# Kernel optimization log

Measured on AMD Instinct MI355X. Metric: run time of the kernel, lower is better.

Reference implementation:

```python
import jax, jax.numpy as jnp
import numpy as np

B, T, D_IN, H, N_CLASSES = 32, 64, 10000, 200, 2


def setup_inputs() -> dict:
    key = jax.random.key(0)
    ks = jax.random.split(key, 16)
    s_in = 1.0 / np.sqrt(H)  # torch nn.RNN init scale
    def u(k, shape):
        return jax.random.uniform(k, shape, jnp.float32, -s_in, s_in)
    inp = {"x": jax.random.normal(ks[0], (B, T, D_IN), jnp.float32)}
    dims = [D_IN, H, H]
    for l in range(3):
        inp[f"W_ih{l}"] = u(ks[1 + 4 * l], (H, dims[l]))
        inp[f"W_hh{l}"] = u(ks[2 + 4 * l], (H, H))
        inp[f"b_ih{l}"] = u(ks[3 + 4 * l], (H,))
        inp[f"b_hh{l}"] = u(ks[4 + 4 * l], (H,))
    inp["fc_w"] = u(ks[13], (N_CLASSES, H))
    inp["fc_b"] = u(ks[14], (N_CLASSES,))
    return inp


def _rnn_layer(x_seq, W_ih, W_hh, b_ih, b_hh):
    # x_seq: [B, T, D] -> hidden sequence [B, T, H]
    pre = jnp.einsum('btd,hd->bth', x_seq, W_ih) + b_ih + b_hh  # input proj batched over time
    h0 = jnp.zeros((x_seq.shape[0], W_hh.shape[0]), x_seq.dtype)

    def step(h, p_t):
        h_new = jnp.tanh(p_t + h @ W_hh.T)
        return h_new, h_new

    _, hs = jax.lax.scan(step, h0, jnp.swapaxes(pre, 0, 1))  # [T, B, H]
    return jnp.swapaxes(hs, 0, 1)


def reference(x, W_ih0, W_hh0, b_ih0, b_hh0, W_ih1, W_hh1, b_ih1, b_hh1,
              W_ih2, W_hh2, b_ih2, b_hh2, fc_w, fc_b):
    h = _rnn_layer(x, W_ih0, W_hh0, b_ih0, b_hh0)
    h = _rnn_layer(h, W_ih1, W_hh1, b_ih1, b_hh1)
    h = _rnn_layer(h, W_ih2, W_hh2, b_ih2, b_hh2)
    last = h[:, -1, :]  # [B, H]; dropout is identity at inference
    logits = last @ fc_w.T + fc_b  # [B, n_classes]
    return logits
```

## Files before the change

kernel.cpp:

```cpp
#include <hip/hip_runtime.h>
#include <hip/hip_bf16.h>


typedef __bf16  bf16x8 __attribute__((ext_vector_type(8)));
typedef __bf16  bf16x4 __attribute__((ext_vector_type(4)));
typedef float   f32x4  __attribute__((ext_vector_type(4)));

#define HDIM 200
#define BM 64
#define CHUNK_B 26624
#define MFMA(a, b, c) __builtin_amdgcn_mfma_f32_16x16x32_bf16(a, b, c, 0, 0, 0)

__device__ __forceinline__ void glds16(const void* g, void* l) {
    __builtin_amdgcn_global_load_lds(
        (const __attribute__((address_space(1))) unsigned int*)g,
        (__attribute__((address_space(3))) unsigned int*)l, 16, 0, 0);
}

__global__ void pack_all(const float* __restrict__ W0,
                         const float* __restrict__ W1,
                         const float* __restrict__ W2,
                         __bf16* __restrict__ O0,
                         __bf16* __restrict__ O1,
                         __bf16* __restrict__ O2)
{
    const int T0 = 320 * 1664, T1 = 7 * 1664, T2 = 7 * 1664;
    for (int gt = blockIdx.x * blockDim.x + threadIdx.x; gt < T0 + T1 + T2;
         gt += gridDim.x * blockDim.x) {
        const float* W; __bf16* out; int K, g;
        if (gt < T0)           { W = W0; out = O0; K = 10000; g = gt; }
        else if (gt < T0 + T1) { W = W1; out = O1; K = HDIM;  g = gt - T0; }
        else                   { W = W2; out = O2; K = HDIM;  g = gt - T0 - T1; }

        const int kc = g / 1664;
        const int u  = g - kc * 1664;
        const int isLo = (u >= 832);
        const int u2 = isLo ? u - 832 : u;
        const int nt = u2 >> 6;
        const int l  = u2 & 63;
        const int r  = nt * 16 + (l & 15);
        const int k  = kc * 32 + (l >> 4) * 8;
        bf16x8 v;
        if (r < HDIM && k < K) {
            const float* p = W + (size_t)r * K + k;
            float4 a = *(const float4*)p, b = *(const float4*)(p + 4);
            float f[8] = {a.x, a.y, a.z, a.w, b.x, b.y, b.z, b.w};
#pragma unroll
            for (int i = 0; i < 8; ++i) {
                __bf16 h = (__bf16)f[i];
                v[i] = isLo ? (__bf16)(f[i] - (float)h) : h;
            }
        } else {
#pragma unroll
            for (int i = 0; i < 8; ++i) v[i] = (__bf16)0.f;
        }
        *(bf16x8*)&out[(size_t)g * 8] = v;
    }
}

__global__ __launch_bounds__(512, 4)
void gemm_pipe(const float* __restrict__ A, int lda, int K,
               const __bf16* __restrict__ Bpack,
               float* __restrict__ Cbase, int per_split, int ksteps)
{
    __shared__ alignas(16) __bf16 Ab[2][4096];
    __shared__ alignas(16) __bf16 Bb[2][13312];

    const int tid = threadIdx.x;
    const int kc0 = blockIdx.y * ksteps;
    const int m0  = blockIdx.x * BM;
    float* __restrict__ C = Cbase + (size_t)blockIdx.y * per_split;

    const int wv = tid >> 6, lane = tid & 63;
    const int r16 = lane & 15, kg = lane >> 4;
    const int mg = wv & 1, ng = wv >> 1;
    const int nt0 = ng ? 1 + ng * 3 : 0;
    const int ntw = ng ? 3 : 4;
    const int fb  = lane * 8;

    const int a_row = tid >> 3;
    const int a_q   = tid & 7;
    const float* Arow = A + (size_t)(m0 + a_row) * lda + a_q * 4;
    const int a_off = (a_row >> 4) * 512 + ((a_row & 15) + 16 * (a_q >> 1)) * 8
                    + (a_q & 1) * 4;

    f32x4 acc[2][4];
#pragma unroll
    for (int mi = 0; mi < 2; ++mi)
#pragma unroll
        for (int j = 0; j < 4; ++j) acc[mi][j] = (f32x4)0.f;

    float av[4];
    auto loadA = [&](int ks) {
        const int kb = (kc0 + ks) * 32;
        if (kb + a_q * 4 < K) {
            float4 x0 = *(const float4*)(Arow + kb);
            av[0] = x0.x; av[1] = x0.y; av[2] = x0.z; av[3] = x0.w;
        } else {
#pragma unroll
            for (int i = 0; i < 4; ++i) av[i] = 0.f;
        }
    };
    auto issueB = [&](int ks, int buf) {
        const char* src = (const char*)Bpack + (size_t)(kc0 + ks) * CHUNK_B;
        char* dst = (char*)&Bb[buf][0];
#pragma unroll
        for (int r = 0; r < 3; ++r)
            glds16(src + (r * 512 + tid) * 16, dst + (r * 512 + tid) * 16);
        if (tid < 128)
            glds16(src + (1536 + tid) * 16, dst + (1536 + tid) * 16);
    };

    loadA(0);
    issueB(0, 0);

    for (int ks = 0; ks < ksteps; ++ks) {
        const int cur = ks & 1, nxt = cur ^ 1;
        bf16x4 th, tl;
#pragma unroll
        for (int i = 0; i < 4; ++i) {
            __bf16 h = (__bf16)av[i];
            th[i] = h; tl[i] = (__bf16)(av[i] - (float)h);
        }
        *(bf16x4*)&Ab[cur][a_off]        = th;
        *(bf16x4*)&Ab[cur][2048 + a_off] = tl;
        __syncthreads();
        if (ks + 1 < ksteps) { issueB(ks + 1, nxt); loadA(ks + 1); }

        const int ao0 = (mg * 2 + 0) * 512 + fb;
        const int ao1 = (mg * 2 + 1) * 512 + fb;
        bf16x8 ah0 = *(const bf16x8*)&Ab[cur][ao0];
        bf16x8 al0 = *(const bf16x8*)&Ab[cur][2048 + ao0];
        bf16x8 ah1 = *(const bf16x8*)&Ab[cur][ao1];
        bf16x8 al1 = *(const bf16x8*)&Ab[cur][2048 + ao1];
#pragma unroll
        for (int j = 0; j < 4; ++j) {
            if (j < ntw) {
                const int bo = (nt0 + j) * 512 + fb;
                bf16x8 bh = *(const bf16x8*)&Bb[cur][bo];
                bf16x8 bl = *(const bf16x8*)&Bb[cur][6656 + bo];
                acc[0][j] = MFMA(al0, bh, acc[0][j]);
                acc[0][j] = MFMA(ah0, bl, acc[0][j]);
                acc[0][j] = MFMA(ah0, bh, acc[0][j]);
                acc[1][j] = MFMA(al1, bh, acc[1][j]);
                acc[1][j] = MFMA(ah1, bl, acc[1][j]);
                acc[1][j] = MFMA(ah1, bh, acc[1][j]);
            }
        }
    }

#pragma unroll
    for (int mi = 0; mi < 2; ++mi) {
        const int rb = m0 + mg * 32 + mi * 16 + kg * 4;
#pragma unroll
        for (int j = 0; j < 4; ++j) {
            if (j < ntw) {
                const int n = (nt0 + j) * 16 + r16;
                if (n < HDIM)
#pragma unroll
                    for (int r = 0; r < 4; ++r)
                        C[(size_t)(rb + r) * HDIM + n] = acc[mi][j][r];
            }
        }
    }
}

__global__ void reduce_parts(const float* __restrict__ Pp, float* __restrict__ P)
{
    const int i = blockIdx.x * blockDim.x + threadIdx.x;
    if (i < 102400) {
        float4 s = ((const float4*)Pp)[i];
#pragma unroll
        for (int r = 1; r < 16; ++r) {
            float4 v = ((const float4*)Pp)[(size_t)r * 102400 + i];
            s.x += v.x; s.y += v.y; s.z += v.z; s.w += v.w;
        }
        ((float4*)P)[i] = s;
    }
}

__device__ __forceinline__ float fast_tanh(float x) {
    float e = __expf(-2.f * fabsf(x));
    float r = (1.f - e) / (1.f + e);
    return copysignf(r, x);
}

__device__ __forceinline__ void bar_lds() {
    asm volatile("s_waitcnt lgkmcnt(0)" ::: "memory");
    __builtin_amdgcn_s_barrier();
}

__global__ __launch_bounds__(512, 1)
void rnn_rec(const float* __restrict__ pre,
             const float* __restrict__ Whh,
             const float* __restrict__ bih,
             const float* __restrict__ bhh,
             float* __restrict__ Hout)
{
    const int b   = blockIdx.x;
    const int tid = threadIdx.x;

    __shared__ float preS[64 * HDIM];
    __shared__ float h[HDIM];
    __shared__ float bias[HDIM];
    __shared__ float part[10][HDIM];

    {
        const float4* ps = (const float4*)(pre + (size_t)b * 64 * HDIM);
        float4* pd = (float4*)preS;
        for (int i = tid; i < 3200; i += 512) pd[i] = ps[i];
    }

    const bool act = tid < 500;
    const int g  = tid / 10;
    const int s  = tid - g * 10;
    const int n0 = g * 4;
    const int k0 = s * 20;

    float w[80];
    if (act) {
#pragma unroll
        for (int j = 0; j < 4; ++j) {
            const float* wr = Whh + (size_t)(n0 + j) * HDIM + k0;
#pragma unroll
            for (int i = 0; i < 5; ++i) {
                float4 v = *(const float4*)(wr + i * 4);
                w[j * 20 + i * 4 + 0] = v.x; w[j * 20 + i * 4 + 1] = v.y;
                w[j * 20 + i * 4 + 2] = v.z; w[j * 20 + i * 4 + 3] = v.w;
            }
        }
    }
    if (tid < HDIM) { bias[tid] = bih[tid] + bhh[tid]; h[tid] = 0.f; }
    __syncthreads();

    for (int t = 0; t < 64; ++t) {
        if (act) {
            float a0 = 0.f, a1 = 0.f, a2 = 0.f, a3 = 0.f;
#pragma unroll
            for (int i = 0; i < 5; ++i) {
                float4 hv = *(const float4*)&h[k0 + i * 4];
                a0 += w[ 0 + i*4]*hv.x + w[ 1 + i*4]*hv.y + w[ 2 + i*4]*hv.z + w[ 3 + i*4]*hv.w;
                a1 += w[20 + i*4]*hv.x + w[21 + i*4]*hv.y + w[22 + i*4]*hv.z + w[23 + i*4]*hv.w;
                a2 += w[40 + i*4]*hv.x + w[41 + i*4]*hv.y + w[42 + i*4]*hv.z + w[43 + i*4]*hv.w;
                a3 += w[60 + i*4]*hv.x + w[61 + i*4]*hv.y + w[62 + i*4]*hv.z + w[63 + i*4]*hv.w;
            }
            float4 pv = make_float4(a0, a1, a2, a3);
            *(float4*)&part[s][n0] = pv;
        }
        bar_lds();
        if (tid < HDIM) {
            float sum = part[0][tid];
#pragma unroll
            for (int r = 1; r < 10; ++r) sum += part[r][tid];
            float v = fast_tanh(sum + preS[t * HDIM + tid] + bias[tid]);
            h[tid] = v;
            Hout[((size_t)b * 64 + t) * HDIM + tid] = v;
        }
        bar_lds();
    }
}

__global__ void fc_head(const float* __restrict__ Hlast_base,
                        const float* __restrict__ fcw,
                        const float* __restrict__ fcb,
                        float* __restrict__ out)
{
    const int i = threadIdx.x;
    if (i >= 64) return;
    const int b = i >> 1, cls = i & 1;
    const float* hp = Hlast_base + ((size_t)b * 64 + 63) * HDIM;
    const float* fw = fcw + cls * HDIM;
    float s = fcb[cls];
    for (int j = 0; j < HDIM; ++j) s += hp[j] * fw[j];
    out[b * 2 + cls] = s;
}

extern "C" void kernel_launch(void* const* d_in, const int* in_sizes, int n_in,
                              void* d_out, int out_size, void* d_ws, size_t ws_size,
                              hipStream_t stream) {
    const float* x     = (const float*)d_in[0];
    const float* W_ih0 = (const float*)d_in[1];
    const float* W_hh0 = (const float*)d_in[2];
    const float* b_ih0 = (const float*)d_in[3];
    const float* b_hh0 = (const float*)d_in[4];
    const float* W_ih1 = (const float*)d_in[5];
    const float* W_hh1 = (const float*)d_in[6];
    const float* b_ih1 = (const float*)d_in[7];
    const float* b_hh1 = (const float*)d_in[8];
    const float* W_ih2 = (const float*)d_in[9];
    const float* W_hh2 = (const float*)d_in[10];
    const float* b_ih2 = (const float*)d_in[11];
    const float* b_hh2 = (const float*)d_in[12];
    const float* fc_w  = (const float*)d_in[13];
    const float* fc_b  = (const float*)d_in[14];
    float* out = (float*)d_out;

    const size_t PE = (size_t)2048 * HDIM;
    float* P     = (float*)d_ws;
    float* Hbuf  = P + PE;
    float* Hbuf2 = Hbuf + PE;
    float* Ppart = Hbuf2 + PE;
    __bf16* W0p  = (__bf16*)(Ppart + 16 * PE);
    __bf16* W1p  = W0p + (size_t)320 * 13312;
    __bf16* W2p  = W1p + (size_t)7 * 13312;

    pack_all<<<1024, 256, 0, stream>>>(W_ih0, W_ih1, W_ih2, W0p, W1p, W2p);

    gemm_pipe<<<dim3(32, 16), 512, 0, stream>>>(x, 10000, 10000, W0p, Ppart, (int)PE, 20);
    reduce_parts<<<400, 256, 0, stream>>>(Ppart, P);
    rnn_rec<<<32, 512, 0, stream>>>(P, W_hh0, b_ih0, b_hh0, Hbuf);

    gemm_pipe<<<dim3(32, 1), 512, 0, stream>>>(Hbuf, HDIM, HDIM, W1p, P, (int)PE, 7);
    rnn_rec<<<32, 512, 0, stream>>>(P, W_hh1, b_ih1, b_hh1, Hbuf2);

    gemm_pipe<<<dim3(32, 1), 512, 0, stream>>>(Hbuf2, HDIM, HDIM, W2p, P, (int)PE, 7);
    rnn_rec<<<32, 512, 0, stream>>>(P, W_hh2, b_ih2, b_hh2, Hbuf);

    fc_head<<<1, 64, 0, stream>>>(Hbuf, fc_w, fc_b, out);
}
```

Before: 315.5 us.

## Replace split-K partial buffers with atomic accumulation and load A fragments directly

The split-K layer-0 GEMM now accumulates its 16 partial results into P with float atomicAdd. P is zeroed inside the pack kernel, which removes the 16x partial-sum buffer and the separate reduce kernel. The A operand is no longer staged through LDS: each lane loads its own fp32 fragment from global memory and splits it into bf16 hi/lo in registers. This frees LDS and removes the LDS write and read for A. The cost is contended atomics on P, non-deterministic summation order, and redundant A loads across the wave groups that share rows.

```diff
diff --git a/kernel.cpp b/kernel.cpp
--- a/kernel.cpp
+++ b/kernel.cpp
@@ -3,7 +3,6 @@
 
 
 typedef __bf16  bf16x8 __attribute__((ext_vector_type(8)));
-typedef __bf16  bf16x4 __attribute__((ext_vector_type(4)));
 typedef float   f32x4  __attribute__((ext_vector_type(4)));
 
 #define HDIM 200
@@ -22,8 +21,15 @@
                          const float* __restrict__ W2,
                          __bf16* __restrict__ O0,
                          __bf16* __restrict__ O1,
-                         __bf16* __restrict__ O2)
+                         __bf16* __restrict__ O2,
+                         float* __restrict__ P)
 {
+    {
+        const float4 z = make_float4(0.f, 0.f, 0.f, 0.f);
+        for (int i = blockIdx.x * blockDim.x + threadIdx.x; i < 102400;
+             i += gridDim.x * blockDim.x)
+            ((float4*)P)[i] = z;
+    }
     const int T0 = 320 * 1664, T1 = 7 * 1664, T2 = 7 * 1664;
     for (int gt = blockIdx.x * blockDim.x + threadIdx.x; gt < T0 + T1 + T2;
          gt += gridDim.x * blockDim.x) {
@@ -61,15 +67,16 @@
 __global__ __launch_bounds__(512, 4)
 void gemm_pipe(const float* __restrict__ A, int lda, int K,
                const __bf16* __restrict__ Bpack,
-               float* __restrict__ Cbase, int per_split, int ksteps)
+               float* __restrict__ Cbase, int per_split, int ksteps,
+               int atomic_out)
 {
-    __shared__ alignas(16) __bf16 Ab[2][4096];
     __shared__ alignas(16) __bf16 Bb[2][13312];
 
     const int tid = threadIdx.x;
     const int kc0 = blockIdx.y * ksteps;
     const int m0  = blockIdx.x * BM;
-    float* __restrict__ C = Cbase + (size_t)blockIdx.y * per_split;
+    float* __restrict__ C = atomic_out ? Cbase
+                          : Cbase + (size_t)blockIdx.y * per_split;
 
     const int wv = tid >> 6, lane = tid & 63;
     const int r16 = lane & 15, kg = lane >> 4;
@@ -78,11 +85,9 @@
     const int ntw = ng ? 3 : 4;
     const int fb  = lane * 8;
 
-    const int a_row = tid >> 3;
-    const int a_q   = tid & 7;
-    const float* Arow = A + (size_t)(m0 + a_row) * lda + a_q * 4;
-    const int a_off = (a_row >> 4) * 512 + ((a_row & 15) + 16 * (a_q >> 1)) * 8
-                    + (a_q & 1) * 4;
+    const int k8 = kg * 8;
+    const float* Ap0 = A + (size_t)(m0 + mg * 32 + r16) * lda + k8;
+    const float* Ap1 = Ap0 + (size_t)16 * lda;
 
     f32x4 acc[2][4];
 #pragma unroll
@@ -90,15 +95,21 @@
 #pragma unroll
         for (int j = 0; j < 4; ++j) acc[mi][j] = (f32x4)0.f;
 
-    float av[4];
+    float af[16];
     auto loadA = [&](int ks) {
         const int kb = (kc0 + ks) * 32;
-        if (kb + a_q * 4 < K) {
-            float4 x0 = *(const float4*)(Arow + kb);
-            av[0] = x0.x; av[1] = x0.y; av[2] = x0.z; av[3] = x0.w;
+        if (kb + k8 < K) {
+            const float* p0 = Ap0 + kb;
+            const float* p1 = Ap1 + kb;
+            float4 a = *(const float4*)p0, b = *(const float4*)(p0 + 4);
+            float4 c = *(const float4*)p1, d = *(const float4*)(p1 + 4);
+            af[0]=a.x; af[1]=a.y; af[2]=a.z; af[3]=a.w;
+            af[4]=b.x; af[5]=b.y; af[6]=b.z; af[7]=b.w;
+            af[8]=c.x; af[9]=c.y; af[10]=c.z; af[11]=c.w;
+            af[12]=d.x; af[13]=d.y; af[14]=d.z; af[15]=d.w;
         } else {
 #pragma unroll
-            for (int i = 0; i < 4; ++i) av[i] = 0.f;
+            for (int i = 0; i < 16; ++i) af[i] = 0.f;
         }
     };
     auto issueB = [&](int ks, int buf) {
@@ -116,23 +127,17 @@
 
     for (int ks = 0; ks < ksteps; ++ks) {
         const int cur = ks & 1, nxt = cur ^ 1;
-        bf16x4 th, tl;
-#pragma unroll
-        for (int i = 0; i < 4; ++i) {
-            __bf16 h = (__bf16)av[i];
-            th[i] = h; tl[i] = (__bf16)(av[i] - (float)h);
-        }
-        *(bf16x4*)&Ab[cur][a_off]        = th;
-        *(bf16x4*)&Ab[cur][2048 + a_off] = tl;
+        bf16x8 ah0, al0, ah1, al1;
+#pragma unroll
+        for (int i = 0; i < 8; ++i) {
+            __bf16 h0 = (__bf16)af[i];
+            ah0[i] = h0; al0[i] = (__bf16)(af[i] - (float)h0);
+            __bf16 h1 = (__bf16)af[8 + i];
+            ah1[i] = h1; al1[i] = (__bf16)(af[8 + i] - (float)h1);
+        }
         __syncthreads();
         if (ks + 1 < ksteps) { issueB(ks + 1, nxt); loadA(ks + 1); }
 
-        const int ao0 = (mg * 2 + 0) * 512 + fb;
-        const int ao1 = (mg * 2 + 1) * 512 + fb;
-        bf16x8 ah0 = *(const bf16x8*)&Ab[cur][ao0];
-        bf16x8 al0 = *(const bf16x8*)&Ab[cur][2048 + ao0];
-        bf16x8 ah1 = *(const bf16x8*)&Ab[cur][ao1];
-        bf16x8 al1 = *(const bf16x8*)&Ab[cur][2048 + ao1];
 #pragma unroll
         for (int j = 0; j < 4; ++j) {
             if (j < ntw) {
@@ -156,26 +161,20 @@
         for (int j = 0; j < 4; ++j) {
             if (j < ntw) {
                 const int n = (nt0 + j) * 16 + r16;
-                if (n < HDIM)
-#pragma unroll
-                    for (int r = 0; r < 4; ++r)
-                        C[(size_t)(rb + r) * HDIM + n] = acc[mi][j][r];
-            }
-        }
-    }
-}
-
-__global__ void reduce_parts(const float* __restrict__ Pp, float* __restrict__ P)
-{
-    const int i = blockIdx.x * blockDim.x + threadIdx.x;
-    if (i < 102400) {
-        float4 s = ((const float4*)Pp)[i];
-#pragma unroll
-        for (int r = 1; r < 16; ++r) {
-            float4 v = ((const float4*)Pp)[(size_t)r * 102400 + i];
-            s.x += v.x; s.y += v.y; s.z += v.z; s.w += v.w;
-        }
-        ((float4*)P)[i] = s;
+                if (n < HDIM) {
+                    if (atomic_out) {
+#pragma unroll
+                        for (int r = 0; r < 4; ++r)
+                            atomicAdd(&C[(size_t)(rb + r) * HDIM + n],
+                                      acc[mi][j][r]);
+                    } else {
+#pragma unroll
+                        for (int r = 0; r < 4; ++r)
+                            C[(size_t)(rb + r) * HDIM + n] = acc[mi][j][r];
+                    }
+                }
+            }
+        }
     }
 }
 
@@ -299,21 +298,19 @@
     float* P     = (float*)d_ws;
     float* Hbuf  = P + PE;
     float* Hbuf2 = Hbuf + PE;
-    float* Ppart = Hbuf2 + PE;
-    __bf16* W0p  = (__bf16*)(Ppart + 16 * PE);
+    __bf16* W0p  = (__bf16*)(Hbuf2 + PE);
     __bf16* W1p  = W0p + (size_t)320 * 13312;
     __bf16* W2p  = W1p + (size_t)7 * 13312;
 
-    pack_all<<<1024, 256, 0, stream>>>(W_ih0, W_ih1, W_ih2, W0p, W1p, W2p);
-
-    gemm_pipe<<<dim3(32, 16), 512, 0, stream>>>(x, 10000, 10000, W0p, Ppart, (int)PE, 20);
-    reduce_parts<<<400, 256, 0, stream>>>(Ppart, P);
+    pack_all<<<1024, 256, 0, stream>>>(W_ih0, W_ih1, W_ih2, W0p, W1p, W2p, P);
+
+    gemm_pipe<<<dim3(32, 16), 512, 0, stream>>>(x, 10000, 10000, W0p, P, (int)PE, 20, 1);
     rnn_rec<<<32, 512, 0, stream>>>(P, W_hh0, b_ih0, b_hh0, Hbuf);
 
-    gemm_pipe<<<dim3(32, 1), 512, 0, stream>>>(Hbuf, HDIM, HDIM, W1p, P, (int)PE, 7);
+    gemm_pipe<<<dim3(32, 1), 512, 0, stream>>>(Hbuf, HDIM, HDIM, W1p, P, (int)PE, 7, 0);
     rnn_rec<<<32, 512, 0, stream>>>(P, W_hh1, b_ih1, b_hh1, Hbuf2);
 
-    gemm_pipe<<<dim3(32, 1), 512, 0, stream>>>(Hbuf2, HDIM, HDIM, W2p, P, (int)PE, 7);
+    gemm_pipe<<<dim3(32, 1), 512, 0, stream>>>(Hbuf2, HDIM, HDIM, W2p, P, (int)PE, 7, 0);
     rnn_rec<<<32, 512, 0, stream>>>(P, W_hh2, b_ih2, b_hh2, Hbuf);
 
     fc_head<<<1, 64, 0, stream>>>(Hbuf, fc_w, fc_b, out);
```

After: 348.0 us. +10.3%, slower.

## Fuse all stages into one cooperative persistent kernel with grid syncs

Applied to the files above, without the earlier changes.

Replaces the nine separate launches (pack, big GEMM, reduce, three recurrences, two small GEMMs, FC head) with a single cooperative kernel. Stages are separated by grid-wide syncs, and shared memory is unioned across stages. This aims to remove per-launch overhead and inter-kernel gaps. In exchange it adds grid-sync cost, raises per-block LDS use, which limits occupancy, and runs the GEMM at a different occupancy than its original launch bounds.

```diff
diff --git a/kernel.cpp b/kernel.cpp
--- a/kernel.cpp
+++ b/kernel.cpp
@@ -1,5 +1,8 @@
 #include <hip/hip_runtime.h>
 #include <hip/hip_bf16.h>
+#include <hip/hip_cooperative_groups.h>
+
+namespace cg = cooperative_groups;
 
 
 typedef __bf16  bf16x8 __attribute__((ext_vector_type(8)));
@@ -17,60 +20,34 @@
         (__attribute__((address_space(3))) unsigned int*)l, 16, 0, 0);
 }
 
-__global__ void pack_all(const float* __restrict__ W0,
-                         const float* __restrict__ W1,
-                         const float* __restrict__ W2,
-                         __bf16* __restrict__ O0,
-                         __bf16* __restrict__ O1,
-                         __bf16* __restrict__ O2)
+__device__ __forceinline__ float fast_tanh(float x) {
+    float e = __expf(-2.f * fabsf(x));
+    float r = (1.f - e) / (1.f + e);
+    return copysignf(r, x);
+}
+
+__device__ __forceinline__ void bar_lds() {
+    asm volatile("s_waitcnt lgkmcnt(0)" ::: "memory");
+    __builtin_amdgcn_s_barrier();
+}
+
+struct MegaArgs {
+    const float *x;
+    const float *Wih0, *Whh0, *bih0, *bhh0;
+    const float *Wih1, *Whh1, *bih1, *bhh1;
+    const float *Wih2, *Whh2, *bih2, *bhh2;
+    const float *fcw, *fcb;
+    float *out;
+    float *P, *Hbuf, *Hbuf2, *Ppart;
+    __bf16 *W0p, *W1p, *W2p;
+};
+
+__device__ __noinline__ void gemm_job(
+    const float* __restrict__ A, int lda, int K,
+    const __bf16* __restrict__ Bpack, float* __restrict__ C,
+    int ksteps, int kc0, int m0,
+    __bf16* Ab, __bf16* Bb, int tid)
 {
-    const int T0 = 320 * 1664, T1 = 7 * 1664, T2 = 7 * 1664;
-    for (int gt = blockIdx.x * blockDim.x + threadIdx.x; gt < T0 + T1 + T2;
-         gt += gridDim.x * blockDim.x) {
-        const float* W; __bf16* out; int K, g;
-        if (gt < T0)           { W = W0; out = O0; K = 10000; g = gt; }
-        else if (gt < T0 + T1) { W = W1; out = O1; K = HDIM;  g = gt - T0; }
-        else                   { W = W2; out = O2; K = HDIM;  g = gt - T0 - T1; }
-
-        const int kc = g / 1664;
-        const int u  = g - kc * 1664;
-        const int isLo = (u >= 832);
-        const int u2 = isLo ? u - 832 : u;
-        const int nt = u2 >> 6;
-        const int l  = u2 & 63;
-        const int r  = nt * 16 + (l & 15);
-        const int k  = kc * 32 + (l >> 4) * 8;
-        bf16x8 v;
-        if (r < HDIM && k < K) {
-            const float* p = W + (size_t)r * K + k;
-            float4 a = *(const float4*)p, b = *(const float4*)(p + 4);
-            float f[8] = {a.x, a.y, a.z, a.w, b.x, b.y, b.z, b.w};
-#pragma unroll
-            for (int i = 0; i < 8; ++i) {
-                __bf16 h = (__bf16)f[i];
-                v[i] = isLo ? (__bf16)(f[i] - (float)h) : h;
-            }
-        } else {
-#pragma unroll
-            for (int i = 0; i < 8; ++i) v[i] = (__bf16)0.f;
-        }
-        *(bf16x8*)&out[(size_t)g * 8] = v;
-    }
-}
-
-__global__ __launch_bounds__(512, 4)
-void gemm_pipe(const float* __restrict__ A, int lda, int K,
-               const __bf16* __restrict__ Bpack,
-               float* __restrict__ Cbase, int per_split, int ksteps)
-{
-    __shared__ alignas(16) __bf16 Ab[2][4096];
-    __shared__ alignas(16) __bf16 Bb[2][13312];
-
-    const int tid = threadIdx.x;
-    const int kc0 = blockIdx.y * ksteps;
-    const int m0  = blockIdx.x * BM;
-    float* __restrict__ C = Cbase + (size_t)blockIdx.y * per_split;
-
     const int wv = tid >> 6, lane = tid & 63;
     const int r16 = lane & 15, kg = lane >> 4;
     const int mg = wv & 1, ng = wv >> 1;
@@ -103,7 +80,7 @@
     };
     auto issueB = [&](int ks, int buf) {
         const char* src = (const char*)Bpack + (size_t)(kc0 + ks) * CHUNK_B;
-        char* dst = (char*)&Bb[buf][0];
+        char* dst = (char*)Bb + (size_t)buf * CHUNK_B;
 #pragma unroll
         for (int r = 0; r < 3; ++r)
             glds16(src + (r * 512 + tid) * 16, dst + (r * 512 + tid) * 16);
@@ -122,23 +99,23 @@
             __bf16 h = (__bf16)av[i];
             th[i] = h; tl[i] = (__bf16)(av[i] - (float)h);
         }
-        *(bf16x4*)&Ab[cur][a_off]        = th;
-        *(bf16x4*)&Ab[cur][2048 + a_off] = tl;
+        *(bf16x4*)&Ab[cur * 4096 + a_off]        = th;
+        *(bf16x4*)&Ab[cur * 4096 + 2048 + a_off] = tl;
         __syncthreads();
         if (ks + 1 < ksteps) { issueB(ks + 1, nxt); loadA(ks + 1); }
 
         const int ao0 = (mg * 2 + 0) * 512 + fb;
         const int ao1 = (mg * 2 + 1) * 512 + fb;
-        bf16x8 ah0 = *(const bf16x8*)&Ab[cur][ao0];
-        bf16x8 al0 = *(const bf16x8*)&Ab[cur][2048 + ao0];
-        bf16x8 ah1 = *(const bf16x8*)&Ab[cur][ao1];
-        bf16x8 al1 = *(const bf16x8*)&Ab[cur][2048 + ao1];
+        bf16x8 ah0 = *(const bf16x8*)&Ab[cur * 4096 + ao0];
+        bf16x8 al0 = *(const bf16x8*)&Ab[cur * 4096 + 2048 + ao0];
+        bf16x8 ah1 = *(const bf16x8*)&Ab[cur * 4096 + ao1];
+        bf16x8 al1 = *(const bf16x8*)&Ab[cur * 4096 + 2048 + ao1];
 #pragma unroll
         for (int j = 0; j < 4; ++j) {
             if (j < ntw) {
                 const int bo = (nt0 + j) * 512 + fb;
-                bf16x8 bh = *(const bf16x8*)&Bb[cur][bo];
-                bf16x8 bl = *(const bf16x8*)&Bb[cur][6656 + bo];
+                bf16x8 bh = *(const bf16x8*)&Bb[cur * 13312 + bo];
+                bf16x8 bl = *(const bf16x8*)&Bb[cur * 13312 + 6656 + bo];
                 acc[0][j] = MFMA(al0, bh, acc[0][j]);
                 acc[0][j] = MFMA(ah0, bl, acc[0][j]);
                 acc[0][j] = MFMA(ah0, bh, acc[0][j]);
@@ -163,48 +140,16 @@
             }
         }
     }
-}
-
-__global__ void reduce_parts(const float* __restrict__ Pp, float* __restrict__ P)
+    __syncthreads();
+}
+
+__device__ __noinline__ void rec_job(
+    const float* __restrict__ pre, const float* __restrict__ Whh,
+    const float* __restrict__ bih, const float* __restrict__ bhh,
+    float* __restrict__ Hout, int b, int tid,
+    float* __restrict__ preS, float* __restrict__ hS,
+    float* __restrict__ bias, float* __restrict__ part)
 {
-    const int i = blockIdx.x * blockDim.x + threadIdx.x;
-    if (i < 102400) {
-        float4 s = ((const float4*)Pp)[i];
-#pragma unroll
-        for (int r = 1; r < 16; ++r) {
-            float4 v = ((const float4*)Pp)[(size_t)r * 102400 + i];
-            s.x += v.x; s.y += v.y; s.z += v.z; s.w += v.w;
-        }
-        ((float4*)P)[i] = s;
-    }
-}
-
-__device__ __forceinline__ float fast_tanh(float x) {
-    float e = __expf(-2.f * fabsf(x));
-    float r = (1.f - e) / (1.f + e);
-    return copysignf(r, x);
-}
-
-__device__ __forceinline__ void bar_lds() {
-    asm volatile("s_waitcnt lgkmcnt(0)" ::: "memory");
-    __builtin_amdgcn_s_barrier();
-}
-
-__global__ __launch_bounds__(512, 1)
-void rnn_rec(const float* __restrict__ pre,
-             const float* __restrict__ Whh,
-             const float* __restrict__ bih,
-             const float* __restrict__ bhh,
-             float* __restrict__ Hout)
-{
-    const int b   = blockIdx.x;
-    const int tid = threadIdx.x;
-
-    __shared__ float preS[64 * HDIM];
-    __shared__ float h[HDIM];
-    __shared__ float bias[HDIM];
-    __shared__ float part[10][HDIM];
-
     {
         const float4* ps = (const float4*)(pre + (size_t)b * 64 * HDIM);
         float4* pd = (float4*)preS;
@@ -230,7 +175,7 @@
             }
         }
     }
-    if (tid < HDIM) { bias[tid] = bih[tid] + bhh[tid]; h[tid] = 0.f; }
+    if (tid < HDIM) { bias[tid] = bih[tid] + bhh[tid]; hS[tid] = 0.f; }
     __syncthreads();
 
     for (int t = 0; t < 64; ++t) {
@@ -238,83 +183,158 @@
             float a0 = 0.f, a1 = 0.f, a2 = 0.f, a3 = 0.f;
 #pragma unroll
             for (int i = 0; i < 5; ++i) {
-                float4 hv = *(const float4*)&h[k0 + i * 4];
+                float4 hv = *(const float4*)&hS[k0 + i * 4];
                 a0 += w[ 0 + i*4]*hv.x + w[ 1 + i*4]*hv.y + w[ 2 + i*4]*hv.z + w[ 3 + i*4]*hv.w;
                 a1 += w[20 + i*4]*hv.x + w[21 + i*4]*hv.y + w[22 + i*4]*hv.z + w[23 + i*4]*hv.w;
                 a2 += w[40 + i*4]*hv.x + w[41 + i*4]*hv.y + w[42 + i*4]*hv.z + w[43 + i*4]*hv.w;
                 a3 += w[60 + i*4]*hv.x + w[61 + i*4]*hv.y + w[62 + i*4]*hv.z + w[63 + i*4]*hv.w;
             }
             float4 pv = make_float4(a0, a1, a2, a3);
-            *(float4*)&part[s][n0] = pv;
+            *(float4*)&part[s * HDIM + n0] = pv;
         }
         bar_lds();
         if (tid < HDIM) {
-            float sum = part[0][tid];
-#pragma unroll
-            for (int r = 1; r < 10; ++r) sum += part[r][tid];
+            float sum = part[0 * HDIM + tid];
+#pragma unroll
+            for (int r = 1; r < 10; ++r) sum += part[r * HDIM + tid];
             float v = fast_tanh(sum + preS[t * HDIM + tid] + bias[tid]);
-            h[tid] = v;
+            hS[tid] = v;
             Hout[((size_t)b * 64 + t) * HDIM + tid] = v;
         }
         bar_lds();
     }
-}
-
-__global__ void fc_head(const float* __restrict__ Hlast_base,
-                        const float* __restrict__ fcw,
-                        const float* __restrict__ fcb,
-                        float* __restrict__ out)
+    __syncthreads();
+}
+
+__global__ __launch_bounds__(512, 2)
+void mega(MegaArgs a)
 {
-    const int i = threadIdx.x;
-    if (i >= 64) return;
-    const int b = i >> 1, cls = i & 1;
-    const float* hp = Hlast_base + ((size_t)b * 64 + 63) * HDIM;
-    const float* fw = fcw + cls * HDIM;
-    float s = fcb[cls];
-    for (int j = 0; j < HDIM; ++j) s += hp[j] * fw[j];
-    out[b * 2 + cls] = s;
+    __shared__ alignas(16) char U[69632];
+    __bf16* Ab   = (__bf16*)U;
+    __bf16* Bb   = (__bf16*)(U + 16384);
+    float*  preS = (float*)U;
+    float*  hS   = (float*)(U + 51200);
+    float*  bias = (float*)(U + 52000);
+    float*  part = (float*)(U + 52800);
+
+    const int tid = threadIdx.x;
+    const int bid = blockIdx.x;
+    const int nb  = gridDim.x;
+    cg::grid_group grd = cg::this_grid();
+
+    {
+        const int T0 = 320 * 1664, T1 = 7 * 1664, T2 = 7 * 1664;
+        for (int gt = bid * 512 + tid; gt < T0 + T1 + T2; gt += nb * 512) {
+            const float* W; __bf16* outp; int K, g;
+            if (gt < T0)           { W = a.Wih0; outp = a.W0p; K = 10000; g = gt; }
+            else if (gt < T0 + T1) { W = a.Wih1; outp = a.W1p; K = HDIM;  g = gt - T0; }
+            else                   { W = a.Wih2; outp = a.W2p; K = HDIM;  g = gt - T0 - T1; }
+            const int kc = g / 1664;
+            const int u  = g - kc * 1664;
+            const int isLo = (u >= 832);
+            const int u2 = isLo ? u - 832 : u;
+            const int nt = u2 >> 6;
+            const int l  = u2 & 63;
+            const int r  = nt * 16 + (l & 15);
+            const int k  = kc * 32 + (l >> 4) * 8;
+            bf16x8 v;
+            if (r < HDIM && k < K) {
+                const float* p = W + (size_t)r * K + k;
+                float4 aa = *(const float4*)p, bb = *(const float4*)(p + 4);
+                float f[8] = {aa.x, aa.y, aa.z, aa.w, bb.x, bb.y, bb.z, bb.w};
+#pragma unroll
+                for (int i = 0; i < 8; ++i) {
+                    __bf16 h = (__bf16)f[i];
+                    v[i] = isLo ? (__bf16)(f[i] - (float)h) : h;
+                }
+            } else {
+#pragma unroll
+                for (int i = 0; i < 8; ++i) v[i] = (__bf16)0.f;
+            }
+            *(bf16x8*)&outp[(size_t)g * 8] = v;
+        }
+    }
+    grd.sync();
+
+    for (int job = bid; job < 32 * 16; job += nb) {
+        const int mb = job & 31, ys = job >> 5;
+        gemm_job(a.x, 10000, 10000, a.W0p,
+                 a.Ppart + (size_t)ys * (2048 * HDIM),
+                 20, ys * 20, mb * BM, Ab, Bb, tid);
+    }
+    grd.sync();
+
+    for (int i = bid * 512 + tid; i < 102400; i += nb * 512) {
+        float4 s4 = ((const float4*)a.Ppart)[i];
+#pragma unroll
+        for (int r = 1; r < 16; ++r) {
+            float4 v = ((const float4*)a.Ppart)[(size_t)r * 102400 + i];
+            s4.x += v.x; s4.y += v.y; s4.z += v.z; s4.w += v.w;
+        }
+        ((float4*)a.P)[i] = s4;
+    }
+    grd.sync();
+
+    for (int b = bid; b < 32; b += nb)
+        rec_job(a.P, a.Whh0, a.bih0, a.bhh0, a.Hbuf, b, tid, preS, hS, bias, part);
+    grd.sync();
+
+    for (int job = bid; job < 32; job += nb)
+        gemm_job(a.Hbuf, HDIM, HDIM, a.W1p, a.P, 7, 0, job * BM, Ab, Bb, tid);
+    grd.sync();
+
+    for (int b = bid; b < 32; b += nb)
+        rec_job(a.P, a.Whh1, a.bih1, a.bhh1, a.Hbuf2, b, tid, preS, hS, bias, part);
+    grd.sync();
+
+    for (int job = bid; job < 32; job += nb)
+        gemm_job(a.Hbuf2, HDIM, HDIM, a.W2p, a.P, 7, 0, job * BM, Ab, Bb, tid);
+    grd.sync();
+
+    for (int b = bid; b < 32; b += nb)
+        rec_job(a.P, a.Whh2, a.bih2, a.bhh2, a.Hbuf, b, tid, preS, hS, bias, part);
+    grd.sync();
+
+    if (bid == 0 && tid < 64) {
+        const int b = tid >> 1, cls = tid & 1;
+        const float* hp = a.Hbuf + ((size_t)b * 64 + 63) * HDIM;
+        const float* fw = a.fcw + cls * HDIM;
+        float s = a.fcb[cls];
+        for (int j = 0; j < HDIM; ++j) s += hp[j] * fw[j];
+        a.out[b * 2 + cls] = s;
+    }
 }
 
 extern "C" void kernel_launch(void* const* d_in, const int* in_sizes, int n_in,
                               void* d_out, int out_size, void* d_ws, size_t ws_size,
                               hipStream_t stream) {
-    const float* x     = (const float*)d_in[0];
-    const float* W_ih0 = (const float*)d_in[1];
-    const float* W_hh0 = (const float*)d_in[2];
-    const float* b_ih0 = (const float*)d_in[3];
-    const float* b_hh0 = (const float*)d_in[4];
-    const float* W_ih1 = (const float*)d_in[5];
-    const float* W_hh1 = (const float*)d_in[6];
-    const float* b_ih1 = (const float*)d_in[7];
-    const float* b_hh1 = (const float*)d_in[8];
-    const float* W_ih2 = (const float*)d_in[9];
-    const float* W_hh2 = (const float*)d_in[10];
-    const float* b_ih2 = (const float*)d_in[11];
-    const float* b_hh2 = (const float*)d_in[12];
-    const float* fc_w  = (const float*)d_in[13];
-    const float* fc_b  = (const float*)d_in[14];
-    float* out = (float*)d_out;
+    MegaArgs ma;
+    ma.x    = (const float*)d_in[0];
+    ma.Wih0 = (const float*)d_in[1];  ma.Whh0 = (const float*)d_in[2];
+    ma.bih0 = (const float*)d_in[3];  ma.bhh0 = (const float*)d_in[4];
+    ma.Wih1 = (const float*)d_in[5];  ma.Whh1 = (const float*)d_in[6];
+    ma.bih1 = (const float*)d_in[7];  ma.bhh1 = (const float*)d_in[8];
+    ma.Wih2 = (const float*)d_in[9];  ma.Whh2 = (const float*)d_in[10];
+    ma.bih2 = (const float*)d_in[11]; ma.bhh2 = (const float*)d_in[12];
+    ma.fcw  = (const float*)d_in[13]; ma.fcb  = (const float*)d_in[14];
+    ma.out  = (float*)d_out;
 
     const size_t PE = (size_t)2048 * HDIM;
-    float* P     = (float*)d_ws;
-    float* Hbuf  = P + PE;
-    float* Hbuf2 = Hbuf + PE;
-    float* Ppart = Hbuf2 + PE;
-    __bf16* W0p  = (__bf16*)(Ppart + 16 * PE);
-    __bf16* W1p  = W0p + (size_t)320 * 13312;
-    __bf16* W2p  = W1p + (size_t)7 * 13312;
-
-    pack_all<<<1024, 256, 0, stream>>>(W_ih0, W_ih1, W_ih2, W0p, W1p, W2p);
-
-    gemm_pipe<<<dim3(32, 16), 512, 0, stream>>>(x, 10000, 10000, W0p, Ppart, (int)PE, 20);
-    reduce_parts<<<400, 256, 0, stream>>>(Ppart, P);
-    rnn_rec<<<32, 512, 0, stream>>>(P, W_hh0, b_ih0, b_hh0, Hbuf);
-
-    gemm_pipe<<<dim3(32, 1), 512, 0, stream>>>(Hbuf, HDIM, HDIM, W1p, P, (int)PE, 7);
-    rnn_rec<<<32, 512, 0, stream>>>(P, W_hh1, b_ih1, b_hh1, Hbuf2);
-
-    gemm_pipe<<<dim3(32, 1), 512, 0, stream>>>(Hbuf2, HDIM, HDIM, W2p, P, (int)PE, 7);
-    rnn_rec<<<32, 512, 0, stream>>>(P, W_hh2, b_ih2, b_hh2, Hbuf);
-
-    fc_head<<<1, 64, 0, stream>>>(Hbuf, fc_w, fc_b, out);
-}
+    ma.P     = (float*)d_ws;
+    ma.Hbuf  = ma.P + PE;
+    ma.Hbuf2 = ma.Hbuf + PE;
+    ma.Ppart = ma.Hbuf2 + PE;
+    ma.W0p   = (__bf16*)(ma.Ppart + 16 * PE);
+    ma.W1p   = ma.W0p + (size_t)320 * 13312;
+    ma.W2p   = ma.W1p + (size_t)7 * 13312;
+
+    int maxb = 1;
+    hipOccupancyMaxActiveBlocksPerMultiprocessor(&maxb, mega, 512, 0);
+    if (maxb < 1) maxb = 1;
+    int grid = maxb * 256;
+    if (grid > 512) grid = 512;
+
+    void* kargs[] = { (void*)&ma };
+    hipLaunchCooperativeKernel((const void*)mega, dim3(grid), dim3(512),
+                               kargs, 0, stream);
+}
```

Result: slower. 593.7 us (+88.2%).

## Fuse the three recurrent layers, inter-layer GEMMs and FC head into one kernel

Applied to the files above, without the earlier changes.

Replaces the rec/gemm/rec/gemm/rec/fc launch sequence with a single per-batch kernel. Because each block's 64 timesteps map to exactly one 64-row GEMM tile, each block computes its own layer-1/2 input projection in place and reuses a shared LDS union. This removes five kernel launches and their inter-kernel gaps. The cost is a non-inlined GEMM helper, heavier register and LDS pressure, and only 32 blocks running the small GEMMs.

```diff
diff --git a/kernel.cpp b/kernel.cpp
--- a/kernel.cpp
+++ b/kernel.cpp
@@ -15,6 +15,17 @@
     __builtin_amdgcn_global_load_lds(
         (const __attribute__((address_space(1))) unsigned int*)g,
         (__attribute__((address_space(3))) unsigned int*)l, 16, 0, 0);
+}
+
+__device__ __forceinline__ float fast_tanh(float x) {
+    float e = __expf(-2.f * fabsf(x));
+    float r = (1.f - e) / (1.f + e);
+    return copysignf(r, x);
+}
+
+__device__ __forceinline__ void bar_lds() {
+    asm volatile("s_waitcnt lgkmcnt(0)" ::: "memory");
+    __builtin_amdgcn_s_barrier();
 }
 
 __global__ void pack_all(const float* __restrict__ W0,
@@ -58,19 +69,12 @@
     }
 }
 
-__global__ __launch_bounds__(512, 4)
-void gemm_pipe(const float* __restrict__ A, int lda, int K,
-               const __bf16* __restrict__ Bpack,
-               float* __restrict__ Cbase, int per_split, int ksteps)
-{
-    __shared__ alignas(16) __bf16 Ab[2][4096];
-    __shared__ alignas(16) __bf16 Bb[2][13312];
-
-    const int tid = threadIdx.x;
-    const int kc0 = blockIdx.y * ksteps;
-    const int m0  = blockIdx.x * BM;
-    float* __restrict__ C = Cbase + (size_t)blockIdx.y * per_split;
-
+__device__ __noinline__ void gemm_job(
+    const float* __restrict__ A, int lda, int K,
+    const __bf16* __restrict__ Bpack, float* __restrict__ C,
+    int ksteps, int kc0, int m0,
+    __bf16* Ab, __bf16* Bb, int tid)
+{
     const int wv = tid >> 6, lane = tid & 63;
     const int r16 = lane & 15, kg = lane >> 4;
     const int mg = wv & 1, ng = wv >> 1;
@@ -103,7 +107,7 @@
     };
     auto issueB = [&](int ks, int buf) {
         const char* src = (const char*)Bpack + (size_t)(kc0 + ks) * CHUNK_B;
-        char* dst = (char*)&Bb[buf][0];
+        char* dst = (char*)Bb + (size_t)buf * CHUNK_B;
 #pragma unroll
         for (int r = 0; r < 3; ++r)
             glds16(src + (r * 512 + tid) * 16, dst + (r * 512 + tid) * 16);
@@ -122,23 +126,23 @@
             __bf16 h = (__bf16)av[i];
             th[i] = h; tl[i] = (__bf16)(av[i] - (float)h);
         }
-        *(bf16x4*)&Ab[cur][a_off]        = th;
-        *(bf16x4*)&Ab[cur][2048 + a_off] = tl;
+        *(bf16x4*)&Ab[cur * 4096 + a_off]        = th;
+        *(bf16x4*)&Ab[cur * 4096 + 2048 + a_off] = tl;
         __syncthreads();
         if (ks + 1 < ksteps) { issueB(ks + 1, nxt); loadA(ks + 1); }
 
         const int ao0 = (mg * 2 + 0) * 512 + fb;
         const int ao1 = (mg * 2 + 1) * 512 + fb;
-        bf16x8 ah0 = *(const bf16x8*)&Ab[cur][ao0];
-        bf16x8 al0 = *(const bf16x8*)&Ab[cur][2048 + ao0];
-        bf16x8 ah1 = *(const bf16x8*)&Ab[cur][ao1];
-        bf16x8 al1 = *(const bf16x8*)&Ab[cur][2048 + ao1];
+        bf16x8 ah0 = *(const bf16x8*)&Ab[cur * 4096 + ao0];
+        bf16x8 al0 = *(const bf16x8*)&Ab[cur * 4096 + 2048 + ao0];
+        bf16x8 ah1 = *(const bf16x8*)&Ab[cur * 4096 + ao1];
+        bf16x8 al1 = *(const bf16x8*)&Ab[cur * 4096 + 2048 + ao1];
 #pragma unroll
         for (int j = 0; j < 4; ++j) {
             if (j < ntw) {
                 const int bo = (nt0 + j) * 512 + fb;
-                bf16x8 bh = *(const bf16x8*)&Bb[cur][bo];
-                bf16x8 bl = *(const bf16x8*)&Bb[cur][6656 + bo];
+                bf16x8 bh = *(const bf16x8*)&Bb[cur * 13312 + bo];
+                bf16x8 bl = *(const bf16x8*)&Bb[cur * 13312 + 6656 + bo];
                 acc[0][j] = MFMA(al0, bh, acc[0][j]);
                 acc[0][j] = MFMA(ah0, bl, acc[0][j]);
                 acc[0][j] = MFMA(ah0, bh, acc[0][j]);
@@ -163,6 +167,18 @@
             }
         }
     }
+    __syncthreads();
+}
+
+__global__ __launch_bounds__(512, 4)
+void gemm_l0(const float* __restrict__ x, const __bf16* __restrict__ W0p,
+             float* __restrict__ Ppart, int per_split)
+{
+    __shared__ alignas(16) char U[69632];
+    gemm_job(x, 10000, 10000, W0p,
+             Ppart + (size_t)blockIdx.y * per_split,
+             20, blockIdx.y * 20, blockIdx.x * BM,
+             (__bf16*)U, (__bf16*)(U + 16384), threadIdx.x);
 }
 
 __global__ void reduce_parts(const float* __restrict__ Pp, float* __restrict__ P)
@@ -179,100 +195,111 @@
     }
 }
 
-__device__ __forceinline__ float fast_tanh(float x) {
-    float e = __expf(-2.f * fabsf(x));
-    float r = (1.f - e) / (1.f + e);
-    return copysignf(r, x);
-}
-
-__device__ __forceinline__ void bar_lds() {
-    asm volatile("s_waitcnt lgkmcnt(0)" ::: "memory");
-    __builtin_amdgcn_s_barrier();
-}
-
 __global__ __launch_bounds__(512, 1)
-void rnn_rec(const float* __restrict__ pre,
-             const float* __restrict__ Whh,
-             const float* __restrict__ bih,
-             const float* __restrict__ bhh,
-             float* __restrict__ Hout)
+void rnn_chain(float* P, float* Hbuf,
+               const float* __restrict__ Whh0, const float* __restrict__ bih0,
+               const float* __restrict__ bhh0,
+               const float* __restrict__ Whh1, const float* __restrict__ bih1,
+               const float* __restrict__ bhh1,
+               const float* __restrict__ Whh2, const float* __restrict__ bih2,
+               const float* __restrict__ bhh2,
+               const __bf16* __restrict__ W1p, const __bf16* __restrict__ W2p,
+               const float* __restrict__ fcw, const float* __restrict__ fcb,
+               float* __restrict__ outp)
 {
     const int b   = blockIdx.x;
     const int tid = threadIdx.x;
 
-    __shared__ float preS[64 * HDIM];
-    __shared__ float h[HDIM];
-    __shared__ float bias[HDIM];
-    __shared__ float part[10][HDIM];
-
-    {
-        const float4* ps = (const float4*)(pre + (size_t)b * 64 * HDIM);
-        float4* pd = (float4*)preS;
-        for (int i = tid; i < 3200; i += 512) pd[i] = ps[i];
-    }
-
-    const bool act = tid < 500;
-    const int g  = tid / 10;
-    const int s  = tid - g * 10;
-    const int n0 = g * 4;
-    const int k0 = s * 20;
-
-    float w[80];
-    if (act) {
-#pragma unroll
-        for (int j = 0; j < 4; ++j) {
-            const float* wr = Whh + (size_t)(n0 + j) * HDIM + k0;
-#pragma unroll
-            for (int i = 0; i < 5; ++i) {
-                float4 v = *(const float4*)(wr + i * 4);
-                w[j * 20 + i * 4 + 0] = v.x; w[j * 20 + i * 4 + 1] = v.y;
-                w[j * 20 + i * 4 + 2] = v.z; w[j * 20 + i * 4 + 3] = v.w;
-            }
-        }
-    }
-    if (tid < HDIM) { bias[tid] = bih[tid] + bhh[tid]; h[tid] = 0.f; }
+    __shared__ alignas(16) char U[69632];
+    __bf16* Ab   = (__bf16*)U;
+    __bf16* Bb   = (__bf16*)(U + 16384);
+    float*  preS = (float*)U;
+    float*  hS   = (float*)(U + 51200);
+    float*  bias = (float*)(U + 52000);
+    float*  part = (float*)(U + 52800);
+
+    auto rec = [&](const float* pre, const float* Whh, const float* bih,
+                   const float* bhh, float* Hout) {
+        {
+            const float4* ps = (const float4*)(pre + (size_t)b * 64 * HDIM);
+            float4* pd = (float4*)preS;
+            for (int i = tid; i < 3200; i += 512) pd[i] = ps[i];
+        }
+
+        const bool act = tid < 500;
+        const int g  = tid / 10;
+        const int s  = tid - g * 10;
+        const int n0 = g * 4;
+        const int k0 = s * 20;
+
+        float w[80];
+        if (act) {
+#pragma unroll
+            for (int j = 0; j < 4; ++j) {
+                const float* wr = Whh + (size_t)(n0 + j) * HDIM + k0;
+#pragma unroll
+                for (int i = 0; i < 5; ++i) {
+                    float4 v = *(const float4*)(wr + i * 4);
+                    w[j * 20 + i * 4 + 0] = v.x; w[j * 20 + i * 4 + 1] = v.y;
+                    w[j * 20 + i * 4 + 2] = v.z; w[j * 20 + i * 4 + 3] = v.w;
+                }
+            }
+        }
+        if (tid < HDIM) { bias[tid] = bih[tid] + bhh[tid]; hS[tid] = 0.f; }
+        __syncthreads();
+
+        for (int t = 0; t < 64; ++t) {
+            if (act) {
+                float a0 = 0.f, a1 = 0.f, a2 = 0.f, a3 = 0.f;
+#pragma unroll
+                for (int i = 0; i < 5; ++i) {
+                    float4 hv = *(const float4*)&hS[k0 + i * 4];
+                    a0 += w[ 0 + i*4]*hv.x + w[ 1 + i*4]*hv.y + w[ 2 + i*4]*hv.z + w[ 3 + i*4]*hv.w;
+                    a1 += w[20 + i*4]*hv.x + w[21 + i*4]*hv.y + w[22 + i*4]*hv.z + w[23 + i*4]*hv.w;
+                    a2 += w[40 + i*4]*hv.x + w[41 + i*4]*hv.y + w[42 + i*4]*hv.z + w[43 + i*4]*hv.w;
+                    a3 += w[60 + i*4]*hv.x + w[61 + i*4]*hv.y + w[62 + i*4]*hv.z + w[63 + i*4]*hv.w;
+                }
+                float4 pv = make_float4(a0, a1, a2, a3);
+                *(float4*)&part[s * HDIM + n0] = pv;
+            }
+            bar_lds();
+            if (tid < HDIM) {
+                float sum = part[0 * HDIM + tid];
+#pragma unroll
+                for (int r = 1; r < 10; ++r) sum += part[r * HDIM + tid];
+                float v = fast_tanh(sum + preS[t * HDIM + tid] + bias[tid]);
+                hS[tid] = v;
+                Hout[((size_t)b * 64 + t) * HDIM + tid] = v;
+            }
+            bar_lds();
+        }
+    };
+
+    float* Hslab = Hbuf + (size_t)b * 64 * HDIM;
+    float* Pslab = P + (size_t)b * 64 * HDIM;
+
+    rec(P, Whh0, bih0, bhh0, Hbuf);
     __syncthreads();
-
-    for (int t = 0; t < 64; ++t) {
-        if (act) {
-            float a0 = 0.f, a1 = 0.f, a2 = 0.f, a3 = 0.f;
-#pragma unroll
-            for (int i = 0; i < 5; ++i) {
-                float4 hv = *(const float4*)&h[k0 + i * 4];
-                a0 += w[ 0 + i*4]*hv.x + w[ 1 + i*4]*hv.y + w[ 2 + i*4]*hv.z + w[ 3 + i*4]*hv.w;
-                a1 += w[20 + i*4]*hv.x + w[21 + i*4]*hv.y + w[22 + i*4]*hv.z + w[23 + i*4]*hv.w;
-                a2 += w[40 + i*4]*hv.x + w[41 + i*4]*hv.y + w[42 + i*4]*hv.z + w[43 + i*4]*hv.w;
-                a3 += w[60 + i*4]*hv.x + w[61 + i*4]*hv.y + w[62 + i*4]*hv.z + w[63 + i*4]*hv.w;
-            }
-            float4 pv = make_float4(a0, a1, a2, a3);
-            *(float4*)&part[s][n0] = pv;
-        }
-        bar_lds();
-        if (tid < HDIM) {
-            float sum = part[0][tid];
-#pragma unroll
-            for (int r = 1; r < 10; ++r) sum += part[r][tid];
-            float v = fast_tanh(sum + preS[t * HDIM + tid] + bias[tid]);
-            h[tid] = v;
-            Hout[((size_t)b * 64 + t) * HDIM + tid] = v;
-        }
-        bar_lds();
-    }
-}
-
-__global__ void fc_head(const float* __restrict__ Hlast_base,
-                        const float* __restrict__ fcw,
-                        const float* __restrict__ fcb,
-                        float* __restrict__ out)
-{
-    const int i = threadIdx.x;
-    if (i >= 64) return;
-    const int b = i >> 1, cls = i & 1;
-    const float* hp = Hlast_base + ((size_t)b * 64 + 63) * HDIM;
-    const float* fw = fcw + cls * HDIM;
-    float s = fcb[cls];
-    for (int j = 0; j < HDIM; ++j) s += hp[j] * fw[j];
-    out[b * 2 + cls] = s;
+    gemm_job(Hslab, HDIM, HDIM, W1p, Pslab, 7, 0, 0, Ab, Bb, tid);
+
+    rec(P, Whh1, bih1, bhh1, Hbuf);
+    __syncthreads();
+    gemm_job(Hslab, HDIM, HDIM, W2p, Pslab, 7, 0, 0, Ab, Bb, tid);
+
+    rec(P, Whh2, bih2, bhh2, Hbuf);
+
+    if (tid < 16) {
+        const int cls = tid & 1, sl = tid >> 1;
+        const float* fw = fcw + cls * HDIM + sl * 25;
+        const float* hp = hS + sl * 25;
+        float sacc = 0.f;
+#pragma unroll
+        for (int j = 0; j < 25; ++j) sacc += hp[j] * fw[j];
+        sacc += __shfl_xor(sacc, 2);
+        sacc += __shfl_xor(sacc, 4);
+        sacc += __shfl_xor(sacc, 8);
+        if (sl == 0) outp[b * 2 + cls] = sacc + fcb[cls];
+    }
 }
 
 extern "C" void kernel_launch(void* const* d_in, const int* in_sizes, int n_in,
@@ -298,23 +325,17 @@
     const size_t PE = (size_t)2048 * HDIM;
     float* P     = (float*)d_ws;
     float* Hbuf  = P + PE;
-    float* Hbuf2 = Hbuf + PE;
-    float* Ppart = Hbuf2 + PE;
+    float* Ppart = Hbuf + PE;
     __bf16* W0p  = (__bf16*)(Ppart + 16 * PE);
     __bf16* W1p  = W0p + (size_t)320 * 13312;
     __bf16* W2p  = W1p + (size_t)7 * 13312;
 
     pack_all<<<1024, 256, 0, stream>>>(W_ih0, W_ih1, W_ih2, W0p, W1p, W2p);
-
-    gemm_pipe<<<dim3(32, 16), 512, 0, stream>>>(x, 10000, 10000, W0p, Ppart, (int)PE, 20);
+    gemm_l0<<<dim3(32, 16), 512, 0, stream>>>(x, W0p, Ppart, (int)PE);
     reduce_parts<<<400, 256, 0, stream>>>(Ppart, P);
-    rnn_rec<<<32, 512, 0, stream>>>(P, W_hh0, b_ih0, b_hh0, Hbuf);
-
-    gemm_pipe<<<dim3(32, 1), 512, 0, stream>>>(Hbuf, HDIM, HDIM, W1p, P, (int)PE, 7);
-    rnn_rec<<<32, 512, 0, stream>>>(P, W_hh1, b_ih1, b_hh1, Hbuf2);
-
-    gemm_pipe<<<dim3(32, 1), 512, 0, stream>>>(Hbuf2, HDIM, HDIM, W2p, P, (int)PE, 7);
-    rnn_rec<<<32, 512, 0, stream>>>(P, W_hh2, b_ih2, b_hh2, Hbuf);
-
-    fc_head<<<1, 64, 0, stream>>>(Hbuf, fc_w, fc_b, out);
-}
+    rnn_chain<<<32, 512, 0, stream>>>(P, Hbuf,
+                                      W_hh0, b_ih0, b_hh0,
+                                      W_hh1, b_ih1, b_hh1,
+                                      W_hh2, b_ih2, b_hh2,
+                                      W1p, W2p, fc_w, fc_b, out);
+}
```

Result: slower. 329.0 us (+4.3%).
